# Performance work log

Measured on AMD Instinct MI355X. Metric: run time of the kernel, lower is better.

## Reference

```python
import jax, jax.numpy as jnp
import numpy as np

B, T, V, D, H, DK = 64, 384, 12, 256, 4, 64

def _ln(x, g, b):
    m = jnp.mean(x, -1, keepdims=True)
    v = jnp.var(x, -1, keepdims=True)
    return (x - m) * jax.lax.rsqrt(v + 1e-5) * g + b

def _grn(x, W1, b1, W2, b2, Wg, bg, lng, lnb, ctx=None, Wc=None, Ws=None, bs=None):
    # eta2 = ELU(fc1(x) + ctx_proj(ctx)); eta1 = fc2(eta2); GLU; residual; LN
    h = x @ W1 + b1
    if ctx is not None:
        h = h + ctx @ Wc
    h = jax.nn.elu(h)
    h = h @ W2 + b2
    g = h @ Wg + bg
    a, gate = jnp.split(g, 2, axis=-1)
    gated = a * jax.nn.sigmoid(gate)
    skip = x if Ws is None else x @ Ws + bs
    return _ln(skip + gated, lng, lnb)

def setup_inputs() -> dict:
    key = jax.random.key(0)
    ks = iter(jax.random.split(key, 48))
    def rn(shape, s=0.02):
        return jax.random.normal(next(ks), shape, jnp.float32) * s
    return {
        'x': jax.random.normal(next(ks), (B, T, V, D), jnp.float32),
        'context': jax.random.normal(next(ks), (B, D), jnp.float32),
        # flattened GRN of VSN: in=V*D, hidden=D, out=V, context=D, skip needed
        'fg_W1': rn((V * D, D)), 'fg_b1': jnp.zeros((D,), jnp.float32),
        'fg_Wc': rn((D, D)),
        'fg_W2': rn((D, D)), 'fg_b2': jnp.zeros((D,), jnp.float32),
        'fg_Wg': rn((D, 2 * V)), 'fg_bg': jnp.zeros((2 * V,), jnp.float32),
        'fg_Ws': rn((V * D, V)), 'fg_bs': jnp.zeros((V,), jnp.float32),
        'fg_lng': jnp.ones((V,), jnp.float32), 'fg_lnb': jnp.zeros((V,), jnp.float32),
        # per-variable GRNs (V of them, in=out=hidden=D, no skip/ctx), stacked
        'sv_W1': rn((V, D, D)), 'sv_b1': jnp.zeros((V, D), jnp.float32),
        'sv_W2': rn((V, D, D)), 'sv_b2': jnp.zeros((V, D), jnp.float32),
        'sv_Wg': rn((V, D, 2 * D)), 'sv_bg': jnp.zeros((V, 2 * D), jnp.float32),
        'sv_lng': jnp.ones((V, D), jnp.float32), 'sv_lnb': jnp.zeros((V, D), jnp.float32),
        # static enrichment GRN: in=out=hidden=D with context
        'en_W1': rn((D, D)), 'en_b1': jnp.zeros((D,), jnp.float32),
        'en_Wc': rn((D, D)),
        'en_W2': rn((D, D)), 'en_b2': jnp.zeros((D,), jnp.float32),
        'en_Wg': rn((D, 2 * D)), 'en_bg': jnp.zeros((2 * D,), jnp.float32),
        'en_lng': jnp.ones((D,), jnp.float32), 'en_lnb': jnp.zeros((D,), jnp.float32),
        # interpretable MHA: per-head Q/K, shared V, output proj
        'Wq': rn((H, D, DK)), 'Wk': rn((H, D, DK)),
        'Wv': rn((D, DK)), 'Wo': rn((DK, D)),
    }

def reference(x, context, fg_W1, fg_b1, fg_Wc, fg_W2, fg_b2, fg_Wg, fg_bg, fg_Ws, fg_bs,
              fg_lng, fg_lnb, sv_W1, sv_b1, sv_W2, sv_b2, sv_Wg, sv_bg, sv_lng, sv_lnb,
              en_W1, en_b1, en_Wc, en_W2, en_b2, en_Wg, en_bg, en_lng, en_lnb,
              Wq, Wk, Wv, Wo):
    b, t, v, d = x.shape
    ctx3 = context[:, None, :]  # broadcast static context over time
    # ---- Variable Selection Network ----
    xf = x.reshape(b, t, v * d)
    w = _grn(xf, fg_W1, fg_b1, fg_W2, fg_b2, fg_Wg, fg_bg, fg_lng, fg_lnb,
             ctx=ctx3, Wc=fg_Wc, Ws=fg_Ws, bs=fg_bs)
    w = jax.nn.softmax(w, axis=-1)  # (b,t,v)
    per_var = jax.vmap(_grn, in_axes=(2, 0, 0, 0, 0, 0, 0, 0, 0), out_axes=2)(
        x, sv_W1, sv_b1, sv_W2, sv_b2, sv_Wg, sv_bg, sv_lng, sv_lnb)  # (b,t,v,d)
    sel = jnp.sum(per_var * w[..., None], axis=2)  # (b,t,d)
    # ---- static enrichment GRN ----
    enr = _grn(sel, en_W1, en_b1, en_W2, en_b2, en_Wg, en_bg, en_lng, en_lnb,
               ctx=ctx3, Wc=en_Wc)
    # ---- interpretable multi-head attention (causal), per-head Q/K, shared V ----
    q = jnp.einsum('btd,hdk->hbtk', enr, Wq)
    k = jnp.einsum('btd,hdk->hbtk', enr, Wk)
    vp = enr @ Wv  # (b,t,dk), shared across heads
    scale = jax.lax.rsqrt(jnp.asarray(DK, jnp.float32))
    scores = jnp.einsum('hbqd,hbkd->hbqk', q, k) * scale
    mask = jnp.triu(jnp.ones((t, t), bool), 1)  # True = masked (future)
    scores = jnp.where(mask, jnp.asarray(-1e9, scores.dtype), scores)
    attn = jax.nn.softmax(scores, axis=-1)
    heads = jnp.einsum('hbqk,bkd->hbqd', attn, vp)
    out = jnp.mean(heads, axis=0) @ Wo  # mean over heads then shared output proj
    return out
```

## Files before the change

### kernel.cpp

```cpp
#include <hip/hip_runtime.h>
#include <hip/hip_bf16.h>
#include <stdint.h>
#include <stddef.h>

typedef __bf16 bf16;
typedef __bf16 bf16x8 __attribute__((ext_vector_type(8)));
typedef float  f32x4  __attribute__((ext_vector_type(4)));

#define BTR 24576
#define EPI_BIAS  1
#define EPI_CVEC  2
#define EPI_ELU   4
#define EPI_ATTN  8
#define EPI_GATE  32
#define EPI_PERM  64

typedef const __attribute__((address_space(1))) void gas_void;
typedef __attribute__((address_space(3))) void sas_void;
__device__ __forceinline__ void gload16(const void* g, void* s) {
  __builtin_amdgcn_global_load_lds((gas_void*)g, (sas_void*)s, 16, 0, 0);
}
template<int N> __device__ __forceinline__ void waitvm() {
  asm volatile("s_waitcnt vmcnt(%0)" :: "n"(N) : "memory");
}

__device__ __forceinline__ int perm512(int n) {
  return (n < 256) ? (((n >> 4) << 5) + (n & 15))
                   : ((((n - 256) >> 4) << 5) + ((n - 256) & 15) + 16);
}

template<int EPI, bool AF32, bool CF32, int KT = 0>
__global__ __launch_bounds__(256, 2)
void gemm_kernel(const void* __restrict__ Av, int lda, long sAh, long sAb,
                 const bf16* __restrict__ Bt, int ldb, long sBh, long sBb,
                 void* __restrict__ Cv, int ldc, long sC,
                 int K, int zdiv,
                 const float* __restrict__ bias, const float* __restrict__ cvec,
                 long sBias)
{
  constexpr int NBUF = (KT > 0) ? (KT / 32) : 2;
  __shared__ __align__(16) bf16 As[NBUF][128 * 32];
  __shared__ __align__(16) bf16 Bs[NBUF][128 * 32];

  const int tid  = threadIdx.x;
  const int wave = tid >> 6, lane = tid & 63;
  const int wr = wave >> 1, wc = wave & 1;
  const int quad = lane >> 4, l16 = lane & 15;

  const int z  = blockIdx.z;
  const int hh = z / zdiv, bb = z % zdiv;
  const float* AbF = nullptr; const bf16* AbH = nullptr;
  if constexpr (AF32) AbF = (const float*)Av + (long)hh * sAh + (long)bb * sAb;
  else                AbH = (const bf16*)Av  + (long)hh * sAh + (long)bb * sAb;
  const bf16* Bb = Bt + (long)hh * sBh + (long)bb * sBb;
  float* CbF = nullptr; bf16* CbH = nullptr;
  if constexpr (CF32) CbF = (float*)Cv + (long)z * sC;
  else                CbH = (bf16*)Cv  + (long)z * sC;

  const int rowBase = blockIdx.y * 128;
  const int colBase = blockIdx.x * 128;

  f32x4 acc[4][4];
#pragma unroll
  for (int i = 0; i < 4; ++i)
#pragma unroll
    for (int j = 0; j < 4; ++j) { acc[i][j][0]=0.f; acc[i][j][1]=0.f; acc[i][j][2]=0.f; acc[i][j][3]=0.f; }

  const int r0 = tid >> 2, kc = tid & 3;
  const int r1 = tid >> 1, kh = (tid & 1) * 16;
  const int arow = (wr * 64 + l16) * 32 + quad * 8;
  const int brow = (wc * 64 + l16) * 32 + quad * 8;

  if constexpr (KT > 0) {
    constexpr int NT = KT / 32;
    char* AsB = (char*)&As[0][0] + wave * 1024;
    char* BsB = (char*)&Bs[0][0] + wave * 1024;
#pragma unroll
    for (int t = 0; t < NT; ++t) {
      const int k0 = t * 32;
      gload16(AbH + (size_t)(rowBase + r0)      * lda + k0 + kc * 8, AsB + t * 8192);
      gload16(AbH + (size_t)(rowBase + 64 + r0) * lda + k0 + kc * 8, AsB + t * 8192 + 4096);
      gload16(Bb  + (size_t)(colBase + r0)      * ldb + k0 + kc * 8, BsB + t * 8192);
      gload16(Bb  + (size_t)(colBase + 64 + r0) * ldb + k0 + kc * 8, BsB + t * 8192 + 4096);
    }
#define FP_TILE(T)                                                                 \
    if constexpr ((T) < NT) {                                                      \
      waitvm<(NT - 1 - (T)) * 4>();                                                \
      __builtin_amdgcn_s_barrier();                                                \
      const bf16* Asc = &As[(T)][0];                                               \
      const bf16* Bsc = &Bs[(T)][0];                                               \
      bf16x8 af[4], bfv[4];                                                        \
      _Pragma("unroll")                                                            \
      for (int mi = 0; mi < 4; ++mi) af[mi]  = *(const bf16x8*)(Asc + arow + mi * 512); \
      _Pragma("unroll")                                                            \
      for (int ni = 0; ni < 4; ++ni) bfv[ni] = *(const bf16x8*)(Bsc + brow + ni * 512); \
      _Pragma("unroll")                                                            \
      for (int mi = 0; mi < 4; ++mi)                                               \
        _Pragma("unroll")                                                          \
        for (int ni = 0; ni < 4; ++ni)                                             \
          acc[mi][ni] = __builtin_amdgcn_mfma_f32_16x16x32_bf16(af[mi], bfv[ni], acc[mi][ni], 0, 0, 0); \
    }
    FP_TILE(0) FP_TILE(1) FP_TILE(2) FP_TILE(3)
    FP_TILE(4) FP_TILE(5) FP_TILE(6) FP_TILE(7)
#undef FP_TILE
  } else {
    char* AsW = (char*)&As[0][0] + wave * 1024;
    char* BsW = (char*)&Bs[0][0] + wave * 1024;
    f32x4 pf0, pf1, pf2, pf3;
    const int nt = K >> 5;
    int cur = 0;

    if constexpr (AF32) {
      const float* p = AbF + (size_t)(rowBase + r1) * lda + kh;
      pf0 = *(const f32x4*)(p);     pf1 = *(const f32x4*)(p + 4);
      pf2 = *(const f32x4*)(p + 8); pf3 = *(const f32x4*)(p + 12);
    } else {
      gload16(AbH + (size_t)(rowBase + r0)      * lda + kc * 8, AsW);
      gload16(AbH + (size_t)(rowBase + 64 + r0) * lda + kc * 8, AsW + 4096);
    }
    gload16(Bb + (size_t)(colBase + r0)      * ldb + kc * 8, BsW);
    gload16(Bb + (size_t)(colBase + 64 + r0) * ldb + kc * 8, BsW + 4096);
    if constexpr (AF32) {
      bf16x8 a0, a1;
#pragma unroll
      for (int e = 0; e < 4; ++e) {
        a0[e] = (bf16)pf0[e]; a0[4 + e] = (bf16)pf1[e];
        a1[e] = (bf16)pf2[e]; a1[4 + e] = (bf16)pf3[e];
      }
      *(bf16x8*)(&As[0][0] + r1 * 32 + kh)     = a0;
      *(bf16x8*)(&As[0][0] + r1 * 32 + kh + 8) = a1;
    }
    __syncthreads();

    for (int t = 0; t < nt; ++t) {
      const int nxt = cur ^ 1;
      if (t + 1 < nt) {
        const int k1 = (t + 1) * 32;
        if constexpr (AF32) {
          const float* p = AbF + (size_t)(rowBase + r1) * lda + k1 + kh;
          pf0 = *(const f32x4*)(p);     pf1 = *(const f32x4*)(p + 4);
          pf2 = *(const f32x4*)(p + 8); pf3 = *(const f32x4*)(p + 12);
        } else {
          gload16(AbH + (size_t)(rowBase + r0)      * lda + k1 + kc * 8, AsW + nxt * 8192);
          gload16(AbH + (size_t)(rowBase + 64 + r0) * lda + k1 + kc * 8, AsW + nxt * 8192 + 4096);
        }
        gload16(Bb + (size_t)(colBase + r0)      * ldb + k1 + kc * 8, BsW + nxt * 8192);
        gload16(Bb + (size_t)(colBase + 64 + r0) * ldb + k1 + kc * 8, BsW + nxt * 8192 + 4096);
      }

      const bf16* Asc = &As[cur][0];
      const bf16* Bsc = &Bs[cur][0];
      bf16x8 af[4], bfv[4];
#pragma unroll
      for (int mi = 0; mi < 4; ++mi) af[mi]  = *(const bf16x8*)(Asc + arow + mi * 512);
#pragma unroll
      for (int ni = 0; ni < 4; ++ni) bfv[ni] = *(const bf16x8*)(Bsc + brow + ni * 512);
#pragma unroll
      for (int mi = 0; mi < 4; ++mi)
#pragma unroll
        for (int ni = 0; ni < 4; ++ni)
          acc[mi][ni] = __builtin_amdgcn_mfma_f32_16x16x32_bf16(af[mi], bfv[ni], acc[mi][ni], 0, 0, 0);

      if constexpr (AF32) {
        if (t + 1 < nt) {
          bf16x8 a0, a1;
#pragma unroll
          for (int e = 0; e < 4; ++e) {
            a0[e] = (bf16)pf0[e]; a0[4 + e] = (bf16)pf1[e];
            a1[e] = (bf16)pf2[e]; a1[4 + e] = (bf16)pf3[e];
          }
          *(bf16x8*)(&As[nxt][0] + r1 * 32 + kh)     = a0;
          *(bf16x8*)(&As[nxt][0] + r1 * 32 + kh + 8) = a1;
        }
      }
      __syncthreads();
      cur = nxt;
    }
  }

  if constexpr (EPI & EPI_GATE) {
    const float* bp = bias + (size_t)z * sBias;
#pragma unroll
    for (int mi = 0; mi < 4; ++mi) {
#pragma unroll
      for (int nj = 0; nj < 2; ++nj) {
        const int ni = nj * 2;
        const int pa = colBase + wc * 64 + ni * 16 + l16;
        const int j  = (colBase >> 1) + wc * 32 + nj * 16 + l16;
        const float ba = bp[pa], bg = bp[pa + 16];
        const int row0 = rowBase + wr * 64 + mi * 16 + quad * 4;
#pragma unroll
        for (int r = 0; r < 4; ++r) {
          float a = acc[mi][ni][r]     + ba;
          float g = acc[mi][ni + 1][r] + bg;
          CbH[(size_t)(row0 + r) * ldc + j] = (bf16)(a / (1.f + __expf(-g)));
        }
      }
    }
    return;
  }
  const int bctx = (EPI & EPI_CVEC) ? (rowBase / 384) : 0;
  const float* bp = (EPI & EPI_BIAS) ? bias + (size_t)z * sBias : nullptr;
#pragma unroll
  for (int mi = 0; mi < 4; ++mi) {
#pragma unroll
    for (int ni = 0; ni < 4; ++ni) {
      const int row0 = rowBase + wr * 64 + mi * 16 + quad * 4;
      const int col  = colBase + wc * 64 + ni * 16 + l16;
      float bv = (EPI & EPI_BIAS) ? bp[col] : 0.f;
      float cv = (EPI & EPI_CVEC) ? cvec[bctx * 256 + col] : 0.f;
#pragma unroll
      for (int r = 0; r < 4; ++r) {
        float v = acc[mi][ni][r] + bv + cv;
        if (EPI & EPI_ELU)  v = v > 0.f ? v : __expf(v) - 1.f;
        if (EPI & EPI_ATTN) { v *= 0.125f; if (col > row0 + r) v = -1e9f; }
        int srow = row0 + r;
        if constexpr (EPI & EPI_PERM) srow = perm512(srow);
        if constexpr (CF32) CbF[(size_t)srow * ldc + col] = v;
        else                CbH[(size_t)srow * ldc + col] = (bf16)v;
      }
    }
  }
}

__global__ __launch_bounds__(256, 2)
void fgwide_kernel(const float* __restrict__ A, const bf16* __restrict__ Bt,
                   bf16* __restrict__ C, const float* __restrict__ bias,
                   const float* __restrict__ cvec)
{
  __shared__ __align__(16) bf16 As[2][64 * 32];
  __shared__ __align__(16) bf16 Bs[2][384 * 32];
  const int tid = threadIdx.x;
  const int wave = tid >> 6, lane = tid & 63;
  const int quad = lane >> 4, l16 = lane & 15;
  const int rowBase = blockIdx.x * 64;

  f32x4 acc[4][6];
#pragma unroll
  for (int i = 0; i < 4; ++i)
#pragma unroll
    for (int j = 0; j < 6; ++j) { acc[i][j][0]=0.f; acc[i][j][1]=0.f; acc[i][j][2]=0.f; acc[i][j][3]=0.f; }

  const int r1 = tid >> 2, kh = (tid & 3) * 8;
  const int arow = l16 * 32 + quad * 8;
  const int brow = (wave * 96 + l16) * 32 + quad * 8;

  char* BsW = (char*)&Bs[0][0] + wave * 1024;

  f32x4 pf0, pf1;
  int cur = 0;

  {
    const float* p = A + (size_t)(rowBase + r1) * 3072 + kh;
    pf0 = *(const f32x4*)(p); pf1 = *(const f32x4*)(p + 4);
#pragma unroll
    for (int c = 0; c < 6; ++c) {
      const int idx = c * 256 + tid, rb = idx >> 2, kc2 = idx & 3;
      gload16(Bt + (size_t)rb * 3072 + kc2 * 8, BsW + c * 4096);
    }
    bf16x8 av;
#pragma unroll
    for (int e = 0; e < 4; ++e) { av[e] = (bf16)pf0[e]; av[4 + e] = (bf16)pf1[e]; }
    *(bf16x8*)(&As[0][0] + r1 * 32 + kh) = av;
  }
  __syncthreads();

  for (int t = 0; t < 96; ++t) {
    const int nxt = cur ^ 1;
    if (t + 1 < 96) {
      const int k1 = (t + 1) * 32;
      const float* p = A + (size_t)(rowBase + r1) * 3072 + k1 + kh;
      pf0 = *(const f32x4*)(p); pf1 = *(const f32x4*)(p + 4);
#pragma unroll
      for (int c = 0; c < 6; ++c) {
        const int idx = c * 256 + tid, rb = idx >> 2, kc2 = idx & 3;
        gload16(Bt + (size_t)rb * 3072 + k1 + kc2 * 8, BsW + nxt * 24576 + c * 4096);
      }
    }

    const bf16* Asc = &As[cur][0];
    const bf16* Bsc = &Bs[cur][0];
    bf16x8 af[4], bfv[6];
#pragma unroll
    for (int mi = 0; mi < 4; ++mi) af[mi]  = *(const bf16x8*)(Asc + arow + mi * 512);
#pragma unroll
    for (int ni = 0; ni < 6; ++ni) bfv[ni] = *(const bf16x8*)(Bsc + brow + ni * 512);
#pragma unroll
    for (int mi = 0; mi < 4; ++mi)
#pragma unroll
      for (int ni = 0; ni < 6; ++ni)
        acc[mi][ni] = __builtin_amdgcn_mfma_f32_16x16x32_bf16(af[mi], bfv[ni], acc[mi][ni], 0, 0, 0);

    if (t + 1 < 96) {
      bf16x8 av;
#pragma unroll
      for (int e = 0; e < 4; ++e) { av[e] = (bf16)pf0[e]; av[4 + e] = (bf16)pf1[e]; }
      *(bf16x8*)(&As[nxt][0] + r1 * 32 + kh) = av;
    }
    __syncthreads();
    cur = nxt;
  }

  const int bctx = rowBase / 384;
#pragma unroll
  for (int mi = 0; mi < 4; ++mi) {
#pragma unroll
    for (int ni = 0; ni < 6; ++ni) {
      const int col = wave * 96 + ni * 16 + l16;
      const bool act = (wave * 96 + ni * 16) < 256;
      const float bv = bias[col];
      const float cv = act ? cvec[bctx * 256 + col] : 0.f;
      const int row0 = rowBase + mi * 16 + quad * 4;
#pragma unroll
      for (int r = 0; r < 4; ++r) {
        float v = acc[mi][ni][r] + bv + cv;
        if (act) v = v > 0.f ? v : __expf(v) - 1.f;
        C[(size_t)(row0 + r) * 384 + col] = (bf16)v;
      }
    }
  }
}

__global__ void prep_kernel(
    const float* fgW1, const float* fgWs, const float* fgW2, const float* fgWg,
    const float* fgb1, const float* fgbs,
    const float* svW1, const float* svWg, const float* svW2,
    const float* enW1, const float* enWg, const float* enW2,
    const float* Wq, const float* Wk, const float* Wv, const float* Wo,
    bf16* fgW1WsT, bf16* fgWgPT, bf16* fgW2C, float* bias384,
    bf16* svW1T, bf16* svWgT, bf16* svW2C,
    bf16* enW1T, bf16* enWgT, bf16* enW2C,
    bf16* WqkvT, bf16* WoT)
{
  long i = (long)blockIdx.x * 256 + threadIdx.x;
  if (i < 1179648) {
    int n = i / 3072, k = i % 3072; float v;
    if (n < 256) v = fgW1[(size_t)k * 256 + n];
    else { int nn = n - 256; v = (nn < 12) ? fgWs[(size_t)k * 12 + nn] : 0.f; }
    fgW1WsT[i] = (bf16)v; return; } i -= 1179648;
  if (i < 32768)  { int n = i >> 8, k = i & 255; fgWgPT[i] = (n < 24) ? (bf16)fgWg[k * 24 + n] : (bf16)0.f; return; } i -= 32768;
  if (i < 65536)  { fgW2C[i] = (bf16)fgW2[i]; return; } i -= 65536;
  if (i < 384)    { bias384[i] = (i < 256) ? fgb1[i] : ((i < 268) ? fgbs[i - 256] : 0.f); return; } i -= 384;
  if (i < 786432) { long v = i >> 16, r = i & 65535; int n = r >> 8, k = r & 255; svW1T[i] = (bf16)svW1[(v << 16) + k * 256 + n]; return; } i -= 786432;
  if (i < 1572864){ long v = i >> 17, r = i & 131071; int n = r >> 8, k = r & 255; svWgT[i] = (bf16)svWg[(v << 17) + k * 512 + n]; return; } i -= 1572864;
  if (i < 786432) { svW2C[i] = (bf16)svW2[i]; return; } i -= 786432;
  if (i < 65536)  { int n = i >> 8, k = i & 255; enW1T[i] = (bf16)enW1[k * 256 + n]; return; } i -= 65536;
  if (i < 131072) { int n = i >> 8, k = i & 255; enWgT[i] = (bf16)enWg[k * 512 + n]; return; } i -= 131072;
  if (i < 65536)  { enW2C[i] = (bf16)enW2[i]; return; } i -= 65536;
  if (i < 163840) { int n = i >> 8, k = i & 255; float val;
                    if (n < 256)      val = Wq[(n >> 6) * 16384 + k * 64 + (n & 63)];
                    else if (n < 512) { int nn = n - 256; val = Wk[(nn >> 6) * 16384 + k * 64 + (nn & 63)]; }
                    else if (n < 576) val = Wv[k * 64 + (n - 512)];
                    else              val = 0.f;
                    WqkvT[i] = (bf16)val; return; } i -= 163840;
  if (i < 16384)  { int n = i >> 6, k = i & 63; WoT[i] = (bf16)Wo[k * 256 + n]; }
}

__global__ void biasfuse_kernel(const float* fgb2, const float* fgWg, const float* fgbg,
                                const float* svb2, const float* svWg, const float* svbg,
                                const float* enb2, const float* enWg, const float* enbg,
                                float* fgBF, float* svBFP, float* enBFP)
{
  int i = blockIdx.x * 256 + threadIdx.x;
  if (i < 128) {
    float s = 0.f;
    if (i < 24) { s = fgbg[i]; for (int k = 0; k < 256; ++k) s += fgb2[k] * fgWg[k * 24 + i]; }
    fgBF[i] = s; return; } i -= 128;
  if (i < 6144) {
    int v = i >> 9, n = i & 511;
    float s = svbg[v * 512 + n];
    const float* W = svWg + (size_t)v * 131072;
    const float* b2 = svb2 + v * 256;
    for (int k = 0; k < 256; ++k) s += b2[k] * W[k * 512 + n];
    svBFP[v * 512 + perm512(n)] = s; return; } i -= 6144;
  if (i < 512) {
    float s = enbg[i];
    for (int k = 0; k < 256; ++k) s += enb2[k] * enWg[k * 512 + i];
    enBFP[perm512(i)] = s; }
}

__global__ void cvec_kernel(const float* __restrict__ ctx, const float* __restrict__ WcFg,
                            const float* __restrict__ WcEn, float* __restrict__ outFg,
                            float* __restrict__ outEn) {
  int b = blockIdx.x, n = threadIdx.x;
  const float* Wc = blockIdx.y ? WcEn : WcFg;
  float* o = blockIdx.y ? outEn : outFg;
  float acc = 0.f;
  for (int d = 0; d < 256; ++d) acc += ctx[b * 256 + d] * Wc[d * 256 + n];
  o[b * 256 + n] = acc;
}

__global__ void lnsm12_kernel(const bf16* __restrict__ B384, const bf16* __restrict__ GP,
                              const float* __restrict__ lng, const float* __restrict__ lnb,
                              float* __restrict__ w) {
  int r = blockIdx.x * 256 + threadIdx.x;
  if (r >= BTR) return;
  float y[12]; float m = 0.f;
#pragma unroll
  for (int j = 0; j < 12; ++j) {
    float a = (float)GP[(size_t)r * 128 + j];
    float g = (float)GP[(size_t)r * 128 + 12 + j];
    float gated = a / (1.f + __expf(-g));
    y[j] = (float)B384[(size_t)r * 384 + 256 + j] + gated; m += y[j];
  }
  m *= (1.f / 12.f);
  float var = 0.f;
#pragma unroll
  for (int j = 0; j < 12; ++j) { float d = y[j] - m; var += d * d; }
  var *= (1.f / 12.f);
  float rstd = rsqrtf(var + 1e-5f);
  float mx = -1e30f;
#pragma unroll
  for (int j = 0; j < 12; ++j) { y[j] = (y[j] - m) * rstd * lng[j] + lnb[j]; mx = fmaxf(mx, y[j]); }
  float s = 0.f;
#pragma unroll
  for (int j = 0; j < 12; ++j) { y[j] = __expf(y[j] - mx); s += y[j]; }
  float inv = 1.f / s;
#pragma unroll
  for (int j = 0; j < 12; ++j) w[r * 12 + j] = y[j] * inv;
}

__device__ __forceinline__ void block_sum2(float a, float b, float& oa, float& ob) {
#pragma unroll
  for (int o = 32; o; o >>= 1) { a += __shfl_xor(a, o); b += __shfl_xor(b, o); }
  __shared__ float ra[4], rb[4];
  int w = threadIdx.x >> 6;
  if ((threadIdx.x & 63) == 0) { ra[w] = a; rb[w] = b; }
  __syncthreads();
  oa = ra[0] + ra[1] + ra[2] + ra[3];
  ob = rb[0] + rb[1] + rb[2] + rb[3];
  __syncthreads();
}

__global__ __launch_bounds__(256)
void selacc4_kernel(const bf16* __restrict__ GATED, const float* __restrict__ x,
                    const float* __restrict__ w, const float* __restrict__ lng,
                    const float* __restrict__ lnb, float* __restrict__ sel,
                    bf16* __restrict__ selb, int v0, int isFirst, int isLast) {
  int r = blockIdx.x, d = threadIdx.x;
  float acc = isFirst ? 0.f : sel[(size_t)r * 256 + d];
#pragma unroll
  for (int vv = 0; vv < 4; ++vv) {
    int v = v0 + vv;
    float gated = (float)GATED[(size_t)vv * ((size_t)BTR * 256) + (size_t)r * 256 + d];
    float y = x[(size_t)r * 3072 + v * 256 + d] + gated;
    float s1, s2;
    block_sum2(y, y * y, s1, s2);
    float mean = s1 * (1.f / 256.f);
    float var  = s2 * (1.f / 256.f) - mean * mean;
    float val  = (y - mean) * rsqrtf(var + 1e-5f) * lng[v * 256 + d] + lnb[v * 256 + d];
    acc += w[r * 12 + v] * val;
  }
  if (isLast) selb[(size_t)r * 256 + d] = (bf16)acc;
  else        sel[(size_t)r * 256 + d] = acc;
}

__global__ __launch_bounds__(256)
void enrln_kernel(const bf16* __restrict__ GATED, const bf16* __restrict__ skip,
                  const float* __restrict__ lng, const float* __restrict__ lnb,
                  bf16* __restrict__ out) {
  int r = blockIdx.x, d = threadIdx.x;
  float gated = (float)GATED[(size_t)r * 256 + d];
  float y = (float)skip[(size_t)r * 256 + d] + gated;
  float s1, s2;
  block_sum2(y, y * y, s1, s2);
  float mean = s1 * (1.f / 256.f);
  float var = s2 * (1.f / 256.f) - mean * mean;
  float norm = (y - mean) * rsqrtf(var + 1e-5f);
  out[(size_t)r * 256 + d] = (bf16)(norm * lng[d] + lnb[d]);
}

__global__ __launch_bounds__(256)
void softmax_avg_kernel(const bf16* __restrict__ S, bf16* __restrict__ P) {
  const int wv = threadIdx.x >> 6, lane = threadIdx.x & 63;
  const int bq = blockIdx.x * 4 + wv;
  const int b = bq / 384, q = bq % 384;
  float pb[6];
#pragma unroll
  for (int e = 0; e < 6; ++e) pb[e] = 0.f;
  for (int h = 0; h < 4; ++h) {
    const bf16* row = S + ((size_t)((h * 64 + b) * 384 + q)) * 384;
    float v[6]; float m = -1e30f;
#pragma unroll
    for (int e = 0; e < 6; ++e) { v[e] = (float)row[lane + e * 64]; m = fmaxf(m, v[e]); }
#pragma unroll
    for (int o = 32; o; o >>= 1) m = fmaxf(m, __shfl_xor(m, o));
    float l = 0.f;
#pragma unroll
    for (int e = 0; e < 6; ++e) { v[e] = __expf(v[e] - m); l += v[e]; }
#pragma unroll
    for (int o = 32; o; o >>= 1) l += __shfl_xor(l, o);
    float inv = 1.f / l;
#pragma unroll
    for (int e = 0; e < 6; ++e) pb[e] += v[e] * inv;
  }
  bf16* out = P + (size_t)bq * 384;
#pragma unroll
  for (int e = 0; e < 6; ++e) out[lane + e * 64] = (bf16)(0.25f * pb[e]);
}

template<int EPI, bool AF32, bool CF32, int KT = 0>
static inline void rungemm(hipStream_t s,
    const void* A, int lda, const bf16* Bt, int ldb, void* C, int ldc,
    int M, int N, int K,
    const float* bias = nullptr, const float* cvec = nullptr,
    int Z = 1, int zdiv = 1,
    long sAh = 0, long sAb = 0, long sBh = 0, long sBb = 0, long sC = 0, long sBias = 0)
{
  dim3 grid(N / 128, M / 128, Z);
  gemm_kernel<EPI, AF32, CF32, KT><<<grid, 256, 0, s>>>(A, lda, sAh, sAb, Bt, ldb, sBh, sBb, C, ldc, sC, K, zdiv, bias, cvec, sBias);
}

extern "C" void kernel_launch(void* const* d_in, const int* in_sizes, int n_in,
                              void* d_out, int out_size, void* d_ws, size_t ws_size,
                              hipStream_t stream)
{
  (void)in_sizes; (void)n_in; (void)out_size;
  const float* x      = (const float*)d_in[0];
  const float* ctx    = (const float*)d_in[1];
  const float* fg_W1  = (const float*)d_in[2];
  const float* fg_b1  = (const float*)d_in[3];
  const float* fg_Wc  = (const float*)d_in[4];
  const float* fg_W2  = (const float*)d_in[5];
  const float* fg_b2  = (const float*)d_in[6];
  const float* fg_Wg  = (const float*)d_in[7];
  const float* fg_bg  = (const float*)d_in[8];
  const float* fg_Ws  = (const float*)d_in[9];
  const float* fg_bs  = (const float*)d_in[10];
  const float* fg_lng = (const float*)d_in[11];
  const float* fg_lnb = (const float*)d_in[12];
  const float* sv_W1  = (const float*)d_in[13];
  const float* sv_b1  = (const float*)d_in[14];
  const float* sv_W2  = (const float*)d_in[15];
  const float* sv_b2  = (const float*)d_in[16];
  const float* sv_Wg  = (const float*)d_in[17];
  const float* sv_bg  = (const float*)d_in[18];
  const float* sv_lng = (const float*)d_in[19];
  const float* sv_lnb = (const float*)d_in[20];
  const float* en_W1  = (const float*)d_in[21];
  const float* en_b1  = (const float*)d_in[22];
  const float* en_Wc  = (const float*)d_in[23];
  const float* en_W2  = (const float*)d_in[24];
  const float* en_b2  = (const float*)d_in[25];
  const float* en_Wg  = (const float*)d_in[26];
  const float* en_bg  = (const float*)d_in[27];
  const float* en_lng = (const float*)d_in[28];
  const float* en_lnb = (const float*)d_in[29];
  const float* Wq     = (const float*)d_in[30];
  const float* Wk     = (const float*)d_in[31];
  const float* Wv     = (const float*)d_in[32];
  const float* Wo     = (const float*)d_in[33];

  static constexpr size_t OFF_FGW1WST = 0;
  static constexpr size_t OFF_FGWGPT  = OFF_FGW1WST + 2359296;
  static constexpr size_t OFF_FGW2C   = OFF_FGWGPT  + 65536;
  static constexpr size_t OFF_FGW2GT  = OFF_FGW2C   + 131072;
  static constexpr size_t OFF_BIAS384 = OFF_FGW2GT  + 65536;
  static constexpr size_t OFF_FGBF    = OFF_BIAS384 + 1536;
  static constexpr size_t OFF_SVW1T   = OFF_FGBF    + 512;
  static constexpr size_t OFF_SVWGT   = OFF_SVW1T   + 1572864;
  static constexpr size_t OFF_SVW2C   = OFF_SVWGT   + 3145728;
  static constexpr size_t OFF_SVW2GPT = OFF_SVW2C   + 1572864;
  static constexpr size_t OFF_SVBFP   = OFF_SVW2GPT + 3145728;
  static constexpr size_t OFF_ENW1T   = OFF_SVBFP   + 24576;
  static constexpr size_t OFF_ENWGT   = OFF_ENW1T   + 131072;
  static constexpr size_t OFF_ENW2C   = OFF_ENWGT   + 262144;
  static constexpr size_t OFF_ENW2GPT = OFF_ENW2C   + 131072;
  static constexpr size_t OFF_ENBFP   = OFF_ENW2GPT + 262144;
  static constexpr size_t OFF_WQKVT   = OFF_ENBFP   + 2048;
  static constexpr size_t OFF_WOT     = OFF_WQKVT   + 327680;
  static constexpr size_t OFF_CVECFG  = OFF_WOT     + 32768;
  static constexpr size_t OFF_CVECEN  = OFF_CVECFG  + 65536;
  static constexpr size_t ARENA       = OFF_CVECEN  + 65536;
  static constexpr size_t WS_NEEDED = ARENA + 152174592;

  if (ws_size < WS_NEEDED) return;

  char* ws = (char*)d_ws;
  bf16*  fgW1WsT = (bf16*)(ws + OFF_FGW1WST);
  bf16*  fgWgPT  = (bf16*)(ws + OFF_FGWGPT);
  bf16*  fgW2C   = (bf16*)(ws + OFF_FGW2C);
  bf16*  fgW2gT  = (bf16*)(ws + OFF_FGW2GT);
  float* bias384 = (float*)(ws + OFF_BIAS384);
  float* fgBF    = (float*)(ws + OFF_FGBF);
  bf16*  svW1T   = (bf16*)(ws + OFF_SVW1T);
  bf16*  svWgT   = (bf16*)(ws + OFF_SVWGT);
  bf16*  svW2C   = (bf16*)(ws + OFF_SVW2C);
  bf16*  svW2gPT = (bf16*)(ws + OFF_SVW2GPT);
  float* svBFP   = (float*)(ws + OFF_SVBFP);
  bf16*  enW1T   = (bf16*)(ws + OFF_ENW1T);
  bf16*  enWgT   = (bf16*)(ws + OFF_ENWGT);
  bf16*  enW2C   = (bf16*)(ws + OFF_ENW2C);
  bf16*  enW2gPT = (bf16*)(ws + OFF_ENW2GPT);
  float* enBFP   = (float*)(ws + OFF_ENBFP);
  bf16*  WqkvT   = (bf16*)(ws + OFF_WQKVT);
  bf16*  WoT     = (bf16*)(ws + OFF_WOT);
  float* cvecFg  = (float*)(ws + OFF_CVECFG);
  float* cvecEn  = (float*)(ws + OFF_CVECEN);
  char*  ar      = ws + ARENA;
  float* sel     = (float*)(ar + 0);
  bf16*  selb    = (bf16*)(ar + 25165824);
  float* wbuf    = (float*)(ar + 37748736);
  bf16*  H1G     = (bf16*)(ar + 38928384);
  bf16*  BUF384  = (bf16*)(ar + 38928384);
  bf16*  GPAD    = (bf16*)(ar + 57802752);
  bf16*  H1EN    = (bf16*)(ar + 38928384);
  bf16*  GATED   = (bf16*)(ar + 89260032);
  bf16*  GATEDEN = (bf16*)(ar + 89260032);
  bf16*  enr     = (bf16*)(ar + 139591680);
  bf16*  QKV     = (bf16*)(ar + 0);
  bf16*  Pbar    = (bf16*)(ar + 38928384);
  bf16*  Sbuf    = (bf16*)(ar + 64094208);
  bf16*  UT      = (bf16*)(ar + 64094208);
  float* out     = (float*)d_out;

  prep_kernel<<<19010, 256, 0, stream>>>(fg_W1, fg_Ws, fg_W2, fg_Wg, fg_b1, fg_bs,
                                         sv_W1, sv_Wg, sv_W2, en_W1, en_Wg, en_W2,
                                         Wq, Wk, Wv, Wo,
                                         fgW1WsT, fgWgPT, fgW2C, bias384,
                                         svW1T, svWgT, svW2C, enW1T, enWgT, enW2C,
                                         WqkvT, WoT);
  biasfuse_kernel<<<27, 256, 0, stream>>>(fg_b2, fg_Wg, fg_bg, sv_b2, sv_Wg, sv_bg,
                                          en_b2, en_Wg, en_bg, fgBF, svBFP, enBFP);
  cvec_kernel<<<dim3(64, 2), 256, 0, stream>>>(ctx, fg_Wc, en_Wc, cvecFg, cvecEn);

  rungemm<0,        false, false, 256>(stream, fgWgPT, 256, fgW2C, 256, fgW2gT, 256, 128, 256, 256);
  rungemm<EPI_PERM, false, false, 256>(stream, svWgT, 256, svW2C, 256, svW2gPT, 256, 512, 256, 256,
                                       nullptr, nullptr, 12, 12, 0, 131072, 0, 65536, 131072);
  rungemm<EPI_PERM, false, false, 256>(stream, enWgT, 256, enW2C, 256, enW2gPT, 256, 512, 256, 256);

  fgwide_kernel<<<384, 256, 0, stream>>>(x, fgW1WsT, BUF384, bias384, cvecFg);
  rungemm<EPI_BIAS, false, false, 256>(stream, BUF384, 384, fgW2gT, 256, GPAD, 128, BTR, 128, 256, fgBF);
  lnsm12_kernel<<<96, 256, 0, stream>>>(BUF384, GPAD, fg_lng, fg_lnb, wbuf);

  for (int g = 0; g < 3; ++g) {
    rungemm<EPI_BIAS|EPI_ELU, true, false>(
        stream, x + g * 4 * 256, 3072, svW1T + (size_t)g * 4 * 65536, 256, H1G, 256, BTR, 256, 256,
        sv_b1 + g * 4 * 256, nullptr, 4, 4, 0, 256, 0, 65536, (long)BTR * 256, 256);
    rungemm<EPI_BIAS|EPI_GATE, false, false, 256>(
        stream, H1G, 256, svW2gPT + (size_t)g * 4 * 131072, 256, GATED, 256, BTR, 512, 256,
        svBFP + g * 4 * 512, nullptr, 4, 4, 0, (long)BTR * 256, 0, 131072, (long)BTR * 256, 512);
    selacc4_kernel<<<BTR, 256, 0, stream>>>(GATED, x, wbuf, sv_lng, sv_lnb, sel, selb,
                                            g * 4, g == 0, g == 2);
  }

  rungemm<EPI_BIAS|EPI_CVEC|EPI_ELU, false, false, 256>(stream, selb, 256, enW1T, 256, H1EN, 256, BTR, 256, 256, en_b1, cvecEn);
  rungemm<EPI_BIAS|EPI_GATE, false, false, 256>(stream, H1EN, 256, enW2gPT, 256, GATEDEN, 256, BTR, 512, 256, enBFP);
  enrln_kernel<<<BTR, 256, 0, stream>>>(GATEDEN, selb, en_lng, en_lnb, enr);

  rungemm<0, false, false, 256>(stream, enr, 256, WqkvT, 256, QKV, 640, BTR, 640, 256);
  rungemm<EPI_ATTN, false, false, 64>(stream, QKV, 640, QKV + 256, 640, Sbuf, 384, 384, 384, 64,
                                      nullptr, nullptr, 256, 64, 64, 245760L, 64, 245760L, 147456L);
  softmax_avg_kernel<<<6144, 256, 0, stream>>>(Sbuf, Pbar);
  rungemm<0, false, false, 64>(stream, WoT, 64, QKV + 512, 640, UT, 384, 256, 384, 64,
                               nullptr, nullptr, 64, 64, 0, 0, 0, 245760L, 98304L);
  rungemm<0, false, true>(stream, Pbar, 384, UT, 384, out, 256, 384, 256, 384,
                          nullptr, nullptr, 64, 1, 147456L, 0, 98304L, 0, 98304L);
}
```

Baseline: 1.369 ms.

## Remap gemm blocks across XCDs, skip masked attention tiles, shrink fgwide row tile

```diff
diff --git a/kernel.cpp b/kernel.cpp
--- a/kernel.cpp
+++ b/kernel.cpp
@@ -5,6 +5,7 @@
 
 typedef __bf16 bf16;
 typedef __bf16 bf16x8 __attribute__((ext_vector_type(8)));
+typedef __bf16 bf16x4 __attribute__((ext_vector_type(4)));
 typedef float  f32x4  __attribute__((ext_vector_type(4)));
 
 #define BTR 24576
@@ -47,7 +48,19 @@
   const int wr = wave >> 1, wc = wave & 1;
   const int quad = lane >> 4, l16 = lane & 15;
 
-  const int z  = blockIdx.z;
+  const int gx = gridDim.x, gxy = gridDim.x * gridDim.y;
+  const int nwg = gxy * gridDim.z;
+  int lin = (blockIdx.z * gridDim.y + blockIdx.y) * gx + blockIdx.x;
+  {
+    const int q8 = nwg >> 3, r8 = nwg & 7;
+    const int xcd = lin & 7, idx = lin >> 3;
+    lin = (xcd < r8) ? xcd * (q8 + 1) + idx
+                     : r8 * (q8 + 1) + (xcd - r8) * q8 + idx;
+  }
+  const int z  = lin / gxy;
+  const int rem = lin - z * gxy;
+  const int by = rem / gx, bx = rem - by * gx;
+
   const int hh = z / zdiv, bb = z % zdiv;
   const float* AbF = nullptr; const bf16* AbH = nullptr;
   if constexpr (AF32) AbF = (const float*)Av + (long)hh * sAh + (long)bb * sAb;
@@ -57,8 +70,8 @@
   if constexpr (CF32) CbF = (float*)Cv + (long)z * sC;
   else                CbH = (bf16*)Cv  + (long)z * sC;
 
-  const int rowBase = blockIdx.y * 128;
-  const int colBase = blockIdx.x * 128;
+  const int rowBase = by * 128;
+  const int colBase = bx * 128;
 
   f32x4 acc[4][4];
 #pragma unroll
@@ -71,6 +84,9 @@
   const int arow = (wr * 64 + l16) * 32 + quad * 8;
   const int brow = (wc * 64 + l16) * 32 + quad * 8;
 
+  const bool skipK = (EPI & EPI_ATTN) && (colBase > rowBase);
+
+  if (!skipK) {
   if constexpr (KT > 0) {
     constexpr int NT = KT / 32;
     char* AsB = (char*)&As[0][0] + wave * 1024;
@@ -177,6 +193,7 @@
       cur = nxt;
     }
   }
+  }
 
   if constexpr (EPI & EPI_GATE) {
     const float* bp = bias + (size_t)z * sBias;
@@ -223,45 +240,44 @@
   }
 }
 
-__global__ __launch_bounds__(256, 2)
+__global__ __launch_bounds__(256, 3)
 void fgwide_kernel(const float* __restrict__ A, const bf16* __restrict__ Bt,
                    bf16* __restrict__ C, const float* __restrict__ bias,
                    const float* __restrict__ cvec)
 {
-  __shared__ __align__(16) bf16 As[2][64 * 32];
+  __shared__ __align__(16) bf16 As[2][32 * 32];
   __shared__ __align__(16) bf16 Bs[2][384 * 32];
   const int tid = threadIdx.x;
   const int wave = tid >> 6, lane = tid & 63;
   const int quad = lane >> 4, l16 = lane & 15;
-  const int rowBase = blockIdx.x * 64;
-
-  f32x4 acc[4][6];
-#pragma unroll
-  for (int i = 0; i < 4; ++i)
+  const int rowBase = blockIdx.x * 32;
+
+  f32x4 acc[2][6];
+#pragma unroll
+  for (int i = 0; i < 2; ++i)
 #pragma unroll
     for (int j = 0; j < 6; ++j) { acc[i][j][0]=0.f; acc[i][j][1]=0.f; acc[i][j][2]=0.f; acc[i][j][3]=0.f; }
 
-  const int r1 = tid >> 2, kh = (tid & 3) * 8;
+  const int r1 = tid >> 3, kc1 = (tid & 7) * 4;
   const int arow = l16 * 32 + quad * 8;
   const int brow = (wave * 96 + l16) * 32 + quad * 8;
 
   char* BsW = (char*)&Bs[0][0] + wave * 1024;
 
-  f32x4 pf0, pf1;
+  f32x4 pf;
   int cur = 0;
 
   {
-    const float* p = A + (size_t)(rowBase + r1) * 3072 + kh;
-    pf0 = *(const f32x4*)(p); pf1 = *(const f32x4*)(p + 4);
+    pf = *(const f32x4*)(A + (size_t)(rowBase + r1) * 3072 + kc1);
 #pragma unroll
     for (int c = 0; c < 6; ++c) {
       const int idx = c * 256 + tid, rb = idx >> 2, kc2 = idx & 3;
       gload16(Bt + (size_t)rb * 3072 + kc2 * 8, BsW + c * 4096);
     }
-    bf16x8 av;
-#pragma unroll
-    for (int e = 0; e < 4; ++e) { av[e] = (bf16)pf0[e]; av[4 + e] = (bf16)pf1[e]; }
-    *(bf16x8*)(&As[0][0] + r1 * 32 + kh) = av;
+    bf16x4 av;
+#pragma unroll
+    for (int e = 0; e < 4; ++e) av[e] = (bf16)pf[e];
+    *(bf16x4*)(&As[0][0] + r1 * 32 + kc1) = av;
   }
   __syncthreads();
 
@@ -269,8 +285,7 @@
     const int nxt = cur ^ 1;
     if (t + 1 < 96) {
       const int k1 = (t + 1) * 32;
-      const float* p = A + (size_t)(rowBase + r1) * 3072 + k1 + kh;
-      pf0 = *(const f32x4*)(p); pf1 = *(const f32x4*)(p + 4);
+      pf = *(const f32x4*)(A + (size_t)(rowBase + r1) * 3072 + k1 + kc1);
 #pragma unroll
       for (int c = 0; c < 6; ++c) {
         const int idx = c * 256 + tid, rb = idx >> 2, kc2 = idx & 3;
@@ -280,22 +295,22 @@
 
     const bf16* Asc = &As[cur][0];
     const bf16* Bsc = &Bs[cur][0];
-    bf16x8 af[4], bfv[6];
-#pragma unroll
-    for (int mi = 0; mi < 4; ++mi) af[mi]  = *(const bf16x8*)(Asc + arow + mi * 512);
+    bf16x8 af[2], bfv[6];
+#pragma unroll
+    for (int mi = 0; mi < 2; ++mi) af[mi]  = *(const bf16x8*)(Asc + arow + mi * 512);
 #pragma unroll
     for (int ni = 0; ni < 6; ++ni) bfv[ni] = *(const bf16x8*)(Bsc + brow + ni * 512);
 #pragma unroll
-    for (int mi = 0; mi < 4; ++mi)
+    for (int mi = 0; mi < 2; ++mi)
 #pragma unroll
       for (int ni = 0; ni < 6; ++ni)
         acc[mi][ni] = __builtin_amdgcn_mfma_f32_16x16x32_bf16(af[mi], bfv[ni], acc[mi][ni], 0, 0, 0);
 
     if (t + 1 < 96) {
-      bf16x8 av;
-#pragma unroll
-      for (int e = 0; e < 4; ++e) { av[e] = (bf16)pf0[e]; av[4 + e] = (bf16)pf1[e]; }
-      *(bf16x8*)(&As[nxt][0] + r1 * 32 + kh) = av;
+      bf16x4 av;
+#pragma unroll
+      for (int e = 0; e < 4; ++e) av[e] = (bf16)pf[e];
+      *(bf16x4*)(&As[nxt][0] + r1 * 32 + kc1) = av;
     }
     __syncthreads();
     cur = nxt;
@@ -303,7 +318,7 @@
 
   const int bctx = rowBase / 384;
 #pragma unroll
-  for (int mi = 0; mi < 4; ++mi) {
+  for (int mi = 0; mi < 2; ++mi) {
 #pragma unroll
     for (int ni = 0; ni < 6; ++ni) {
       const int col = wave * 96 + ni * 16 + l16;
@@ -629,7 +644,7 @@
                                        nullptr, nullptr, 12, 12, 0, 131072, 0, 65536, 131072);
   rungemm<EPI_PERM, false, false, 256>(stream, enWgT, 256, enW2C, 256, enW2gPT, 256, 512, 256, 256);
 
-  fgwide_kernel<<<384, 256, 0, stream>>>(x, fgW1WsT, BUF384, bias384, cvecFg);
+  fgwide_kernel<<<768, 256, 0, stream>>>(x, fgW1WsT, BUF384, bias384, cvecFg);
   rungemm<EPI_BIAS, false, false, 256>(stream, BUF384, 384, fgW2gT, 256, GPAD, 128, BTR, 128, 256, fgBF);
   lnsm12_kernel<<<96, 256, 0, stream>>>(BUF384, GPAD, fg_lng, fg_lnb, wbuf);
 
```

New measurement: 1.402 ms. 1.02x slower.
